# Kernel optimization log

Measured on AMD Instinct MI355X. Metric: run time of the kernel, lower is better.

## Reference

```python
import jax, jax.numpy as jnp
import numpy as np

DECAY = 0.99
EPS = 1e-05
B, C, H, W = 64, 64, 64, 64   # C == embedding_dim
K = 512                       # num_embedding


def setup_inputs() -> dict:
    key = jax.random.key(0)
    k1, k2 = jax.random.split(key)
    inp = jax.random.normal(k1, (B, C, H, W), dtype=jnp.float32)
    embedding = jax.random.normal(k2, (C, K), dtype=jnp.float32)
    cluster_size = jnp.zeros((K,), dtype=jnp.float32)
    embedding_avg = embedding  # buffer initialized as a clone of embedding
    return {"input": inp, "embedding": embedding,
            "cluster_size": cluster_size, "embedding_avg": embedding_avg}


def reference(input, embedding, cluster_size, embedding_avg):
    # NCHW -> NHWC, flatten to [N, C]
    x = jnp.transpose(input, (0, 2, 3, 1))           # [B,H,W,C]
    flat = x.reshape(-1, embedding.shape[0])          # [N,C]
    # squared L2 distances to all K codes: [N,K]
    dist = (jnp.sum(flat * flat, axis=1, keepdims=True)
            - 2.0 * flat @ embedding
            + jnp.sum(embedding * embedding, axis=0, keepdims=True))
    ind = jnp.argmin(dist, axis=1)                    # [N] int
    # gather codes (uses OLD embedding, as in torch)
    quantize = jnp.take(embedding.T, ind, axis=0).reshape(x.shape)  # [B,H,W,C]
    # EMA updates (training branch). Avoid materializing one-hot:
    counts = jnp.zeros((K,), dtype=flat.dtype).at[ind].add(1.0)      # onehot.sum(0)
    embedding_sum = jax.ops.segment_sum(flat, ind, num_segments=K).T  # [C,K] == flat.T @ onehot
    new_cluster_size = cluster_size * DECAY + (1.0 - DECAY) * counts
    new_embedding_avg = embedding_avg * DECAY + (1.0 - DECAY) * embedding_sum
    n = jnp.sum(new_cluster_size)
    cs = (new_cluster_size + EPS) / (n + K * EPS) * n
    new_embedding = new_embedding_avg / cs[None, :]
    # commitment loss and straight-through estimator
    diff = jnp.mean((jax.lax.stop_gradient(quantize) - x) ** 2)
    quantize_st = x + jax.lax.stop_gradient(quantize - x)
    out = jnp.transpose(quantize_st, (0, 3, 1, 2))    # back to NCHW
    embedding_ind = ind.reshape(x.shape[:-1])         # [B,H,W]
    return out, diff, embedding_ind, new_embedding, new_cluster_size, new_embedding_avg
```

## Files before the change

kernel.cpp:

```cpp
#include <hip/hip_runtime.h>
#include <cstdint>
#include <cstddef>

typedef _Float16 half4v __attribute__((ext_vector_type(4)));
typedef _Float16 half8v __attribute__((ext_vector_type(8)));
typedef float    f32x4  __attribute__((ext_vector_type(4)));

#define N_PTS   262144
#define CDIM    64
#define KCODES  512
#define TAUA    5e-3f
#define FLAG_CAP 65536u
#define STATS_WGS 256

#define OFF_DIFF 16777216u
#define OFF_IND  16777217u
#define OFF_EMB  17039361u
#define OFF_CSZ  17072129u
#define OFF_AVG  17072641u

__global__ __launch_bounds__(512) void k_main(
    const float* __restrict__ in, const float* __restrict__ emb,
    float* __restrict__ out,
    int* __restrict__ ind_buf, float* __restrict__ diff_acc,
    unsigned* __restrict__ nflag, int* __restrict__ flaglist)
{
    __shared__ __align__(16) char bsm[133120];
    float* ee2_lds = (float*)(bsm + 131072);
    const int tid = threadIdx.x;

    {
        const int col = tid;
        const int xr  = (col & 7) << 4;
        float s = 0.f;
        #pragma unroll
        for (int c0 = 0; c0 < CDIM; c0 += 4) {
            float v[4];
            #pragma unroll
            for (int i = 0; i < 4; ++i) v[i] = emb[(c0 + i)*KCODES + col];
            half4v h, lo;
            #pragma unroll
            for (int i = 0; i < 4; ++i) {
                s = fmaf(v[i], v[i], s);
                _Float16 hh = (_Float16)v[i];
                h[i]  = hh;
                lo[i] = (_Float16)(v[i] - (float)hh);
            }
            const int wb = col*128 + ((c0*2) ^ xr);
            *(half4v*)(bsm + wb)         = h;
            *(half4v*)(bsm + 65536 + wb) = lo;
        }
        ee2_lds[col] = 0.5f * s;
    }
    __syncthreads();

    const int w  = tid >> 6, l = tid & 63;
    const int g  = l >> 4,  lc = l & 15;

    for (int r = 0; r < 2; ++r) {
        const int pbase = (blockIdx.x << 10) + (r << 9) + (w << 6);
        const int b     = pbase >> 12;
        const float* inb = in + ((size_t)b << 18) + ((pbase & 4095) + lc);

        half8v ah[4][2], al[4][2];
        float xs = 0.f;
        #pragma unroll
        for (int t = 0; t < 4; ++t)
            #pragma unroll
            for (int s = 0; s < 2; ++s)
                #pragma unroll
                for (int j = 0; j < 8; ++j) {
                    const int c = s*32 + g*8 + j;
                    const float x = inb[(size_t)c*4096 + t*16];
                    xs = fmaf(x, x, xs);
                    const float xf = -x;
                    const _Float16 hh = (_Float16)xf;
                    ah[t][s][j] = hh;
                    al[t][s][j] = (_Float16)(xf - (float)hh);
                }

        float d1[4][4], d2[4][4]; int k1[4][4];
        #pragma unroll
        for (int t = 0; t < 4; ++t)
            #pragma unroll
            for (int rr = 0; rr < 4; ++rr) { d1[t][rr] = 3.4e38f; d2[t][rr] = 3.4e38f; k1[t][rr] = 0; }

        for (int ct = 0; ct < 32; ++ct) {
            const int col  = (ct << 4) + lc;
            const float sd = ee2_lds[col];
            const int rb   = col*128 + ((g*16) ^ ((col & 7) << 4));
            half8v bh0 = *(const half8v*)(bsm + rb);
            half8v bh1 = *(const half8v*)(bsm + (rb ^ 64));
            half8v bl0 = *(const half8v*)(bsm + 65536 + rb);
            half8v bl1 = *(const half8v*)(bsm + 65536 + (rb ^ 64));

            #pragma unroll
            for (int t = 0; t < 4; ++t) {
                f32x4 acc0 = {sd, sd, sd, sd};
                f32x4 acc1 = {0.f, 0.f, 0.f, 0.f};
                acc0 = __builtin_amdgcn_mfma_f32_16x16x32_f16(al[t][0], bh0, acc0, 0, 0, 0);
                acc1 = __builtin_amdgcn_mfma_f32_16x16x32_f16(al[t][1], bh1, acc1, 0, 0, 0);
                acc0 = __builtin_amdgcn_mfma_f32_16x16x32_f16(ah[t][0], bl0, acc0, 0, 0, 0);
                acc1 = __builtin_amdgcn_mfma_f32_16x16x32_f16(ah[t][1], bl1, acc1, 0, 0, 0);
                acc0 = __builtin_amdgcn_mfma_f32_16x16x32_f16(ah[t][0], bh0, acc0, 0, 0, 0);
                acc1 = __builtin_amdgcn_mfma_f32_16x16x32_f16(ah[t][1], bh1, acc1, 0, 0, 0);
                #pragma unroll
                for (int rr = 0; rr < 4; ++rr) {
                    const float d = acc0[rr] + acc1[rr];
                    const bool cc = d < d1[t][rr];
                    d2[t][rr] = fminf(d2[t][rr], fmaxf(d, d1[t][rr]));
                    d1[t][rr] = fminf(d1[t][rr], d);
                    k1[t][rr] = cc ? col : k1[t][rr];
                }
            }
        }

        #pragma unroll
        for (int m = 1; m <= 8; m <<= 1) {
            #pragma unroll
            for (int t = 0; t < 4; ++t)
                #pragma unroll
                for (int rr = 0; rr < 4; ++rr) {
                    const float od1 = __shfl_xor(d1[t][rr], m);
                    const int   ok1 = __shfl_xor(k1[t][rr], m);
                    const float od2 = __shfl_xor(d2[t][rr], m);
                    const float nd2 = fminf(fmaxf(d1[t][rr], od1), fminf(d2[t][rr], od2));
                    const bool take = (od1 < d1[t][rr]) || (od1 == d1[t][rr] && ok1 < k1[t][rr]);
                    d1[t][rr] = take ? od1 : d1[t][rr];
                    k1[t][rr] = take ? ok1 : k1[t][rr];
                    d2[t][rr] = nd2;
                }
        }

        float ds = 0.f;
        if (lc == 0) {
            #pragma unroll
            for (int t = 0; t < 4; ++t) {
                const int nb = pbase + t*16 + (g << 2);
                int4 iv = make_int4(k1[t][0], k1[t][1], k1[t][2], k1[t][3]);
                *(int4*)(ind_buf + nb) = iv;
                #pragma unroll
                for (int rr = 0; rr < 4; ++rr) {
                    ds += d1[t][rr];
                    if (d2[t][rr] - d1[t][rr] < TAUA) {
                        unsigned ix = atomicAdd(nflag, 1u);
                        if (ix < FLAG_CAP) flaglist[ix] = nb + rr;
                    }
                }
            }
        }
        #pragma unroll
        for (int m = 1; m < 64; m <<= 1) {
            ds += __shfl_xor(ds, m);
            xs += __shfl_xor(xs, m);
        }
        if (l == 0) atomicAdd(diff_acc, 2.f*ds + xs);
    }
}

__global__ void k_refine(const float* __restrict__ in, const float* __restrict__ emb,
                         const unsigned* __restrict__ nflag, const int* __restrict__ flaglist,
                         int* __restrict__ ind_buf)
{
    const int gtid = blockIdx.x*blockDim.x + threadIdx.x;
    const int wid  = gtid >> 6;
    const int lane = threadIdx.x & 63;
    const int nw   = (gridDim.x * blockDim.x) >> 6;
    unsigned nf = *nflag; if (nf > FLAG_CAP) nf = FLAG_CAP;
    for (unsigned f = wid; f < nf; f += nw) {
        const int n = flaglist[f];
        const int b = n >> 12, hw = n & 4095;
        const float* xb = in + ((size_t)b << 18) + hw;
        const float* er = emb + lane*8;
        double dd[8] = {0,0,0,0,0,0,0,0};
        for (int c = 0; c < CDIM; ++c) {
            const double xv = (double)xb[(size_t)c << 12];
            #pragma unroll
            for (int j = 0; j < 8; ++j) {
                double t = xv - (double)er[c*KCODES + j];
                dd[j] = fma(t, t, dd[j]);
            }
        }
        double bd = 1e300; int bk = 0;
        #pragma unroll
        for (int j = 0; j < 8; ++j) {
            const int kk = lane*8 + j;
            if (dd[j] < bd) { bd = dd[j]; bk = kk; }
        }
        for (int off = 32; off; off >>= 1) {
            double od = __shfl_xor(bd, off);
            int    ok = __shfl_xor(bk, off);
            if (od < bd || (od == bd && ok < bk)) { bd = od; bk = ok; }
        }
        if (lane == 0) ind_buf[n] = bk;
    }
}

__global__ __launch_bounds__(512) void k_tail(const float* __restrict__ in,
    const float* __restrict__ emb, const int* __restrict__ ind_buf,
    float* __restrict__ p_sum, float* __restrict__ p_cnt, float* __restrict__ out)
{
    __shared__ __align__(16) char xsm[2][CDIM*128];
    __shared__ int   ind_lds[2][32];
    __shared__ float s_cnt[KCODES];

    const int tid = threadIdx.x;

    if (blockIdx.x >= STATS_WGS) {
        const int gid = (blockIdx.x - STATS_WGS)*512 + tid;
        const int i  = gid << 2;
        const int hw = i & 4095;
        const int c  = (i >> 12) & 63;
        const int b  = i >> 18;
        const int n  = (b << 12) + hw;
        const int4 iv = *(const int4*)(ind_buf + n);
        const float* er = emb + (c << 9);
        float4 o = make_float4(er[iv.x], er[iv.y], er[iv.z], er[iv.w]);
        *(float4*)(out + i) = o;
        if (c == 0) {
            out[OFF_IND + n]     = (float)iv.x;
            out[OFF_IND + n + 1] = (float)iv.y;
            out[OFF_IND + n + 2] = (float)iv.z;
            out[OFF_IND + n + 3] = (float)iv.w;
        }
        return;
    }

    const int wg  = blockIdx.x;
    const int n0  = wg << 10;
    const int b   = n0 >> 12;
    const float* inb = in + ((size_t)b << 18) + (n0 & 4095);

    for (int i = tid; i < KCODES; i += 512) s_cnt[i] = 0.f;

    const int sc  = tid >> 3;
    const int sp  = (tid & 7) << 2;
    const int sxr = (sc & 7) << 4;
    const int wb_hi = sc*128 + ((sp*2) ^ sxr);

    const int w  = tid >> 6, l = tid & 63;
    const int g  = l >> 4,  lc = l & 15;
    const int k0w = w << 6;

    f32x4 acc[4][4];
    #pragma unroll
    for (int ci = 0; ci < 4; ++ci)
        #pragma unroll
        for (int kt = 0; kt < 4; ++kt) acc[ci][kt] = (f32x4){0.f, 0.f, 0.f, 0.f};

    {
        const float4 xv = *(const float4*)(inb + (size_t)sc*4096 + sp);
        half4v h;
        #pragma unroll
        for (int i = 0; i < 4; ++i) h[i] = (_Float16)(((const float*)&xv)[i]);
        *(half4v*)(&xsm[0][0] + wb_hi) = h;
        if (tid < 8) *(int4*)&ind_lds[0][tid*4] = *(const int4*)(ind_buf + n0 + tid*4);
    }

    for (int t = 0; t < 32; ++t) {
        __syncthreads();
        float4 nxt; int4 niv;
        if (t < 31) {
            nxt = *(const float4*)(inb + (size_t)sc*4096 + (t+1)*32 + sp);
            if (tid < 8) niv = *(const int4*)(ind_buf + n0 + (t+1)*32 + tid*4);
        }
        if (tid < 32) atomicAdd(&s_cnt[ind_lds[t & 1][tid]], 1.f);

        const char* xb = &xsm[t & 1][0];
        half8v ah[4];
        #pragma unroll
        for (int ci = 0; ci < 4; ++ci) {
            const int c  = (ci << 4) + lc;
            const int xr = (c & 7) << 4;
            ah[ci] = *(const half8v*)(xb + c*128 + ((g*16) ^ xr));
        }
        int idv[8];
        *(int4*)&idv[0] = *(const int4*)&ind_lds[t & 1][g*8];
        *(int4*)&idv[4] = *(const int4*)&ind_lds[t & 1][g*8 + 4];
        #pragma unroll
        for (int kt = 0; kt < 4; ++kt) {
            const int tgt = k0w + (kt << 4) + lc;
            half8v bf;
            #pragma unroll
            for (int j = 0; j < 8; ++j) bf[j] = (idv[j] == tgt) ? (_Float16)1.0f : (_Float16)0.0f;
            #pragma unroll
            for (int ci = 0; ci < 4; ++ci)
                acc[ci][kt] = __builtin_amdgcn_mfma_f32_16x16x32_f16(ah[ci], bf, acc[ci][kt], 0, 0, 0);
        }
        if (t < 31) {
            half4v h;
            #pragma unroll
            for (int i = 0; i < 4; ++i) h[i] = (_Float16)(((const float*)&nxt)[i]);
            *(half4v*)(&xsm[(t+1) & 1][0] + wb_hi) = h;
            if (tid < 8) *(int4*)&ind_lds[(t+1) & 1][tid*4] = niv;
        }
    }
    __syncthreads();

    float* ps = p_sum + (size_t)wg * (CDIM*KCODES);
    #pragma unroll
    for (int ci = 0; ci < 4; ++ci)
        #pragma unroll
        for (int kt = 0; kt < 4; ++kt)
            #pragma unroll
            for (int rr = 0; rr < 4; ++rr)
                ps[((ci << 4) + (g << 2) + rr)*KCODES + k0w + (kt << 4) + lc] = acc[ci][kt][rr];
    float* pc = p_cnt + wg * KCODES;
    for (int i = tid; i < KCODES; i += 512) pc[i] = s_cnt[i];
}

__global__ __launch_bounds__(512) void k_last(const float* __restrict__ p_sum,
    const float* __restrict__ p_cnt, const float* __restrict__ csz,
    const float* __restrict__ eavg, const float* __restrict__ diff_acc,
    float* __restrict__ out)
{
    __shared__ float red[512];
    __shared__ float cs_lds[512];
    const int k = threadIdx.x;
    float c = 0.f;
    for (int w = 0; w < STATS_WGS; ++w) c += p_cnt[w*KCODES + k];
    const float ncs = csz[k]*0.99f + 0.01f*c;
    if (blockIdx.x == 0) out[OFF_CSZ + k] = ncs;
    red[k] = ncs;
    __syncthreads();
    for (int s = 256; s > 0; s >>= 1) { if (k < s) red[k] += red[k+s]; __syncthreads(); }
    const float n = red[0];
    cs_lds[k] = (ncs + 1e-5f) / (n + 0.00512f) * n;
    if (blockIdx.x == 0 && k == 0) out[OFF_DIFF] = diff_acc[0] * (1.f/16777216.f);
    __syncthreads();
    if (k < 256) {
        const int i = blockIdx.x*1024 + k*4;
        float4 s4 = make_float4(0.f, 0.f, 0.f, 0.f);
        for (int w = 0; w < STATS_WGS; ++w) {
            const float4 v = *(const float4*)(p_sum + (size_t)w*(CDIM*KCODES) + i);
            s4.x += v.x; s4.y += v.y; s4.z += v.z; s4.w += v.w;
        }
        const float4 ea = *(const float4*)(eavg + i);
        const float a0 = ea.x*0.99f + 0.01f*s4.x;
        const float a1 = ea.y*0.99f + 0.01f*s4.y;
        const float a2 = ea.z*0.99f + 0.01f*s4.z;
        const float a3 = ea.w*0.99f + 0.01f*s4.w;
        const int kb = i & (KCODES-1);
        out[OFF_AVG + i]     = a0;  out[OFF_AVG + i + 1] = a1;
        out[OFF_AVG + i + 2] = a2;  out[OFF_AVG + i + 3] = a3;
        out[OFF_EMB + i]     = a0 / cs_lds[kb];
        out[OFF_EMB + i + 1] = a1 / cs_lds[kb + 1];
        out[OFF_EMB + i + 2] = a2 / cs_lds[kb + 2];
        out[OFF_EMB + i + 3] = a3 / cs_lds[kb + 3];
    }
}

extern "C" void kernel_launch(void* const* d_in, const int* in_sizes, int n_in,
                              void* d_out, int out_size, void* d_ws, size_t ws_size,
                              hipStream_t stream)
{
    const float* in   = (const float*)d_in[0];
    const float* emb  = (const float*)d_in[1];
    const float* csz  = (const float*)d_in[2];
    const float* eavg = (const float*)d_in[3];
    float* out = (float*)d_out;
    char* ws = (char*)d_ws;

    int*      ind      = (int*)(ws + 2048);
    float*    diff_acc = (float*)(ws + 1050624);
    unsigned* nflag    = (unsigned*)(ws + 1050640);
    int*      flaglist = (int*)(ws + 1050656);
    const size_t off_part = 1447968;
    const int swgs = STATS_WGS;
    float* p_sum = (float*)(ws + off_part);
    float* p_cnt = (float*)(ws + off_part + (size_t)swgs*(CDIM*KCODES)*4);

    hipMemsetAsync(ws + 1050624, 0, 32, stream);

    hipLaunchKernelGGL(k_main,   dim3(256),              dim3(512), 0, stream, in, emb, out, ind, diff_acc, nflag, flaglist);
    hipLaunchKernelGGL(k_refine, dim3(256),              dim3(256), 0, stream, in, emb, nflag, flaglist, ind);
    hipLaunchKernelGGL(k_tail,   dim3(STATS_WGS + 8192), dim3(512), 0, stream, in, emb, ind, p_sum, p_cnt, out);
    hipLaunchKernelGGL(k_last,   dim3(32),               dim3(512), 0, stream, p_sum, p_cnt, csz, eavg, diff_acc, out);
}
```

Before: 194.1 us.

## Atomically accumulate code counts and spread final reduction across more workgroups

```diff
diff --git a/kernel.cpp b/kernel.cpp
--- a/kernel.cpp
+++ b/kernel.cpp
@@ -198,7 +198,7 @@
 
 __global__ __launch_bounds__(512) void k_tail(const float* __restrict__ in,
     const float* __restrict__ emb, const int* __restrict__ ind_buf,
-    float* __restrict__ p_sum, float* __restrict__ p_cnt, float* __restrict__ out)
+    float* __restrict__ p_sum, float* __restrict__ cnt_tot, float* __restrict__ out)
 {
     __shared__ __align__(16) char xsm[2][CDIM*128];
     __shared__ int   ind_lds[2][32];
@@ -305,31 +305,40 @@
             #pragma unroll
             for (int rr = 0; rr < 4; ++rr)
                 ps[((ci << 4) + (g << 2) + rr)*KCODES + k0w + (kt << 4) + lc] = acc[ci][kt][rr];
-    float* pc = p_cnt + wg * KCODES;
-    for (int i = tid; i < KCODES; i += 512) pc[i] = s_cnt[i];
-}
-
-__global__ __launch_bounds__(512) void k_last(const float* __restrict__ p_sum,
-    const float* __restrict__ p_cnt, const float* __restrict__ csz,
+    for (int i = tid; i < KCODES; i += 512) atomicAdd(&cnt_tot[i], s_cnt[i]);
+}
+
+__global__ __launch_bounds__(256) void k_last(const float* __restrict__ p_sum,
+    const float* __restrict__ cnt_tot, const float* __restrict__ csz,
     const float* __restrict__ eavg, const float* __restrict__ diff_acc,
     float* __restrict__ out)
 {
-    __shared__ float red[512];
+    __shared__ float red[256];
+    __shared__ float ncs_lds[512];
     __shared__ float cs_lds[512];
-    const int k = threadIdx.x;
-    float c = 0.f;
-    for (int w = 0; w < STATS_WGS; ++w) c += p_cnt[w*KCODES + k];
-    const float ncs = csz[k]*0.99f + 0.01f*c;
-    if (blockIdx.x == 0) out[OFF_CSZ + k] = ncs;
-    red[k] = ncs;
+    const int tid = threadIdx.x;
+    float part = 0.f;
+    #pragma unroll
+    for (int j = 0; j < 2; ++j) {
+        const int k = j*256 + tid;
+        const float ncs = csz[k]*0.99f + 0.01f*cnt_tot[k];
+        ncs_lds[k] = ncs;
+        part += ncs;
+        if (blockIdx.x == 0) out[OFF_CSZ + k] = ncs;
+    }
+    red[tid] = part;
     __syncthreads();
-    for (int s = 256; s > 0; s >>= 1) { if (k < s) red[k] += red[k+s]; __syncthreads(); }
+    for (int s = 128; s > 0; s >>= 1) { if (tid < s) red[tid] += red[tid+s]; __syncthreads(); }
     const float n = red[0];
-    cs_lds[k] = (ncs + 1e-5f) / (n + 0.00512f) * n;
-    if (blockIdx.x == 0 && k == 0) out[OFF_DIFF] = diff_acc[0] * (1.f/16777216.f);
+    #pragma unroll
+    for (int j = 0; j < 2; ++j) {
+        const int k = j*256 + tid;
+        cs_lds[k] = (ncs_lds[k] + 1e-5f) / (n + 0.00512f) * n;
+    }
+    if (blockIdx.x == 0 && tid == 0) out[OFF_DIFF] = diff_acc[0] * (1.f/16777216.f);
     __syncthreads();
-    if (k < 256) {
-        const int i = blockIdx.x*1024 + k*4;
+    if (tid < 32) {
+        const int i = (blockIdx.x*32 + tid)*4;
         float4 s4 = make_float4(0.f, 0.f, 0.f, 0.f);
         for (int w = 0; w < STATS_WGS; ++w) {
             const float4 v = *(const float4*)(p_sum + (size_t)w*(CDIM*KCODES) + i);
@@ -364,16 +373,15 @@
     int*      ind      = (int*)(ws + 2048);
     float*    diff_acc = (float*)(ws + 1050624);
     unsigned* nflag    = (unsigned*)(ws + 1050640);
-    int*      flaglist = (int*)(ws + 1050656);
+    float*    cnt_tot  = (float*)(ws + 1050656);
+    int*      flaglist = (int*)(ws + 1052704);
     const size_t off_part = 1447968;
-    const int swgs = STATS_WGS;
     float* p_sum = (float*)(ws + off_part);
-    float* p_cnt = (float*)(ws + off_part + (size_t)swgs*(CDIM*KCODES)*4);
-
-    hipMemsetAsync(ws + 1050624, 0, 32, stream);
+
+    hipMemsetAsync(ws + 1050624, 0, 2080, stream);
 
     hipLaunchKernelGGL(k_main,   dim3(256),              dim3(512), 0, stream, in, emb, out, ind, diff_acc, nflag, flaglist);
     hipLaunchKernelGGL(k_refine, dim3(256),              dim3(256), 0, stream, in, emb, nflag, flaglist, ind);
-    hipLaunchKernelGGL(k_tail,   dim3(STATS_WGS + 8192), dim3(512), 0, stream, in, emb, ind, p_sum, p_cnt, out);
-    hipLaunchKernelGGL(k_last,   dim3(32),               dim3(512), 0, stream, p_sum, p_cnt, csz, eavg, diff_acc, out);
-}
+    hipLaunchKernelGGL(k_tail,   dim3(STATS_WGS + 8192), dim3(512), 0, stream, in, emb, ind, p_sum, cnt_tot, out);
+    hipLaunchKernelGGL(k_last,   dim3(256),              dim3(256), 0, stream, p_sum, cnt_tot, csz, eavg, diff_acc, out);
+}
```

Result: faster. 185.5 us (median of 2 runs) (-4.4%).
